# Performance work log

Hardware: AMD Instinct MI355X
Metric: run time of the kernel (lower is better)

## Reference

```python
import jax, jax.numpy as jnp
import numpy as np

NUM_LAYERS = 4
D_MODEL = 128
D_STATE = 16
DELTA_RANK = 8


def setup_inputs() -> dict:
    key = jax.random.key(0)
    ks = jax.random.split(key, 10)
    d, N, dr, L_ = D_MODEL, D_STATE, DELTA_RANK, NUM_LAYERS
    B, R, T = 4, 32, 1024
    x = jax.random.normal(ks[0], (B, R, T), dtype=jnp.float32)

    def w(k, shape, fan_in):
        return jax.random.normal(k, shape, dtype=jnp.float32) / np.sqrt(fan_in).astype(np.float32)

    inp_w = w(ks[1], (d, 1), 1)
    inp_b = jnp.zeros((d,), jnp.float32)
    outp_w = w(ks[2], (1, d), d)
    outp_b = jnp.zeros((1,), jnp.float32)
    ln_g = jnp.ones((L_, d), jnp.float32)
    ln_b = jnp.zeros((L_, d), jnp.float32)
    in_w = w(ks[3], (L_, 2 * d, d), d)
    conv_w = w(ks[4], (L_, d, 3), 3)
    conv_b = jnp.zeros((L_, d), jnp.float32)
    xp_w = w(ks[5], (L_, dr + 2 * N, d), d)
    dp_w = w(ks[6], (L_, d, dr), dr)
    # delta_proj bias = log(dt), dt ~ loguniform(dt_min, dt_max)
    dt = jnp.exp(jax.random.uniform(ks[7], (L_, d), dtype=jnp.float32) * (np.log(0.1) - np.log(0.001)) + np.log(0.001))
    dp_b = jnp.log(dt)
    # A_log = Re(log(-0.5 + i*imag)) = 0.5*log(0.25 + imag^2)
    A_imag = np.arange(1, N + 1, dtype=np.float32) / (1.0 + 2.0 * np.arange(N, dtype=np.float32))
    A_row = 0.5 * np.log(0.25 + A_imag ** 2)
    A_log = jnp.asarray(np.broadcast_to(A_row, (L_, d, N)).copy(), jnp.float32)
    Dp = 0.1 * jnp.ones((L_, d), jnp.float32)
    out_w = w(ks[8], (L_, d, d), d)
    return dict(x=x, inp_w=inp_w, inp_b=inp_b, outp_w=outp_w, outp_b=outp_b,
                ln_g=ln_g, ln_b=ln_b, in_w=in_w, conv_w=conv_w, conv_b=conv_b,
                xp_w=xp_w, dp_w=dp_w, dp_b=dp_b, A_log=A_log, Dp=Dp, out_w=out_w)


def _layernorm(x, g, b):
    mu = jnp.mean(x, -1, keepdims=True)
    v = jnp.var(x, -1, keepdims=True)
    return (x - mu) * jax.lax.rsqrt(v + 1e-5) * g + b


def _selective_scan(u, delta, A_log, Bm, Cm, Dp):
    # u, delta: (Bt, L, d); Bm, Cm: (Bt, L, N); A_log: (d, N); Dp: (d,)
    Bt, L, d = u.shape
    N = A_log.shape[1]
    A = -jnp.exp(A_log)  # (d, N)

    def step(x_prev, inp):
        u_t, dt_t, B_t, C_t = inp  # (Bt,d),(Bt,d),(Bt,N),(Bt,N)
        dA = jnp.exp(dt_t[..., None] * A)                       # (Bt,d,N)
        dBu = dt_t[..., None] * B_t[:, None, :] * u_t[..., None]  # (Bt,d,N)
        x_new = dA * x_prev + dBu
        y_t = jnp.einsum('bdn,bn->bd', x_new, C_t)
        return x_new, y_t

    x0 = jnp.zeros((Bt, d, N), dtype=u.dtype)
    _, ys = jax.lax.scan(step, x0, (u.swapaxes(0, 1), delta.swapaxes(0, 1),
                                    Bm.swapaxes(0, 1), Cm.swapaxes(0, 1)))
    return ys.swapaxes(0, 1) + u * Dp  # (Bt, L, d)


def _block(h, ln_g, ln_b, in_w, conv_w, conv_b, xp_w, dp_w, dp_b, A_log, Dp, out_w):
    Bt, L, d = h.shape
    dr = dp_w.shape[1]
    N = A_log.shape[1]
    z = _layernorm(h, ln_g, ln_b)
    xr = z @ in_w.T                      # (Bt, L, 2d)
    xi, res = jnp.split(xr, 2, axis=-1)
    # depthwise causal conv, kernel=3 (torch pad=2 then crop [:L] == left-pad 2)
    xp = jnp.pad(xi, ((0, 0), (2, 0), (0, 0)))
    xc = (xp[:, 0:L] * conv_w[:, 0] + xp[:, 1:L + 1] * conv_w[:, 1]
          + xp[:, 2:L + 2] * conv_w[:, 2]) + conv_b
    xc = jax.nn.silu(xc)
    dbc = xc @ xp_w.T                    # (Bt, L, dr + 2N)
    dlt, Bm, Cm = jnp.split(dbc, [dr, dr + N], axis=-1)
    delta = jax.nn.softplus(dlt @ dp_w.T + dp_b)  # (Bt, L, d)
    y = _selective_scan(xc, delta, A_log, Bm, Cm, Dp)
    y = y * jax.nn.silu(res)
    return y @ out_w.T


def reference(x, inp_w, inp_b, outp_w, outp_b, ln_g, ln_b, in_w, conv_w, conv_b,
              xp_w, dp_w, dp_b, A_log, Dp, out_w):
    B, R, T = x.shape
    h = x.reshape(B * R, T, 1) @ inp_w.T + inp_b  # (B*R, T, d)
    for i in range(ln_g.shape[0]):
        h = _block(h, ln_g[i], ln_b[i], in_w[i], conv_w[i], conv_b[i], xp_w[i],
                   dp_w[i], dp_b[i], A_log[i], Dp[i], out_w[i]) + h
    out = (h @ outp_w.T + outp_b)[..., 0]  # (B*R, T)
    return out.reshape(B, R, T)
```

## Files before the change

### kernel.cpp

```cpp
#include <hip/hip_runtime.h>
#include <math.h>

#define D 128
#define NSTATE 16
#define DR 8
#define T_SEQ 1024
#define NTOK 131072
#define SEG 16
#define SEGLEN 64
#define ZS 136
#define XRS2 132

typedef __attribute__((ext_vector_type(8))) short bf16x8;
typedef __attribute__((ext_vector_type(4))) float f32x4;

#define LOG2E 1.44269504088896340736f
#define LN2   0.69314718055994530942f

__device__ __forceinline__ float sigmoidf_(float x) {
    return __builtin_amdgcn_rcpf(1.0f + exp2f(-x * LOG2E));
}
__device__ __forceinline__ float softplusf_(float x) {
    float t = LN2 * __builtin_amdgcn_logf(1.0f + exp2f(x * LOG2E));
    return (x > 20.0f) ? x : t;
}
__device__ __forceinline__ short f2bf(float f) {
    union { float f; unsigned u; } v; v.f = f;
    unsigned r = v.u + 0x7FFFu + ((v.u >> 16) & 1u);
    return (short)(r >> 16);
}
__device__ __forceinline__ float bf2f(short s) {
    union { unsigned u; float f; } v; v.u = ((unsigned)(unsigned short)s) << 16;
    return v.f;
}


__global__ void k_prepw(const float* __restrict__ src, short* __restrict__ hi,
                        short* __restrict__ lo, int n) {
    int i = blockIdx.x * 256 + threadIdx.x;
    if (i < n) {
        float f = src[i];
        short hh = f2bf(f);
        hi[i] = hh;
        lo[i] = f2bf(f - bf2f(hh));
    }
}

__global__ void k_prepw_xp(const float* __restrict__ src, short* __restrict__ hi,
                           short* __restrict__ lo) {
    int i = blockIdx.x * 256 + threadIdx.x;
    if (i >= 4 * 48 * 128) return;
    int l = i / (48 * 128);
    int rem = i - l * 48 * 128;
    int j = rem >> 7, k = rem & 127;
    float f = (j < 40) ? src[(l * 40 + j) * 128 + k] : 0.f;
    short hh = f2bf(f);
    hi[i] = hh;
    lo[i] = f2bf(f - bf2f(hh));
}

__global__ void k_a2(const float* __restrict__ A_log, float* __restrict__ A2, int total) {
    int idx = blockIdx.x * blockDim.x + threadIdx.x;
    if (idx < total) A2[idx] = -__expf(A_log[idx]) * LOG2E;
}

__global__ void k_init_h(const float* __restrict__ x, const float* __restrict__ inp_w,
                         const float* __restrict__ inp_b, float* __restrict__ h) {
    int idx = blockIdx.x * blockDim.x + threadIdx.x;
    int tok = idx >> 7;
    int d = idx & 127;
    h[idx] = x[tok] * inp_w[d] + inp_b[d];
}

__global__ __launch_bounds__(256) void k_ln_inproj_conv(
    const float* __restrict__ h, const float* __restrict__ ln_g, const float* __restrict__ ln_b,
    const short* __restrict__ wh, const short* __restrict__ wl,
    const short* __restrict__ xph, const short* __restrict__ xpl,
    const float* __restrict__ conv_w, const float* __restrict__ conv_b,
    float* __restrict__ xc, float* __restrict__ res,
    float* __restrict__ bc, float* __restrict__ dlt)
{
    __shared__ __align__(16) short zsh[48 * ZS];
    __shared__ __align__(16) short zsl[48 * ZS];
    __shared__ __align__(16) float xr[34 * XRS2];
    __shared__ __align__(16) float dbc_l[32][52];
    const int tid = threadIdx.x;
    const int wv = tid >> 6, lane = tid & 63;
    const int tstart = blockIdx.x * 32;
    const int tin = tstart & (T_SEQ - 1);

    for (int r = wv; r < 34; r += 4) {
        int tr = tin + r - 2;
        if (tr < 0) {
            zsh[r * ZS + lane] = 0; zsh[r * ZS + lane + 64] = 0;
            zsl[r * ZS + lane] = 0; zsl[r * ZS + lane + 64] = 0;
            continue;
        }
        size_t row = (size_t)(tstart + r - 2) * D;
        float a = h[row + lane];
        float b = h[row + lane + 64];
        float s = a + b, ss = a * a + b * b;
        #pragma unroll
        for (int m = 1; m < 64; m <<= 1) { s += __shfl_xor(s, m); ss += __shfl_xor(ss, m); }
        float mu = s * (1.0f / 128.0f);
        float var = ss * (1.0f / 128.0f) - mu * mu;
        float rstd = rsqrtf(var + 1e-5f);
        float z0 = (a - mu) * rstd * ln_g[lane]      + ln_b[lane];
        float z1 = (b - mu) * rstd * ln_g[lane + 64] + ln_b[lane + 64];
        short h0 = f2bf(z0), h1 = f2bf(z1);
        zsh[r * ZS + lane]      = h0;
        zsh[r * ZS + lane + 64] = h1;
        zsl[r * ZS + lane]      = f2bf(z0 - bf2f(h0));
        zsl[r * ZS + lane + 64] = f2bf(z1 - bf2f(h1));
    }
    for (int i = tid; i < 14 * 128; i += 256) {
        int r = 34 + (i >> 7), c = i & 127;
        zsh[r * ZS + c] = 0;
        zsl[r * ZS + c] = 0;
    }

    const int colb = wv * 64 + (lane & 15);
    const int kb = (lane >> 4) * 8;
    bf16x8 bw[4][4];
    #pragma unroll
    for (int ct = 0; ct < 4; ++ct)
        #pragma unroll
        for (int kf = 0; kf < 4; ++kf)
            bw[ct][kf] = *(const bf16x8*)&wh[(colb + ct * 16) * 128 + kf * 32 + kb];
    __syncthreads();

    f32x4 acc[3][4];
    #pragma unroll
    for (int b = 0; b < 3; ++b)
        #pragma unroll
        for (int ct = 0; ct < 4; ++ct)
            acc[b][ct] = (f32x4){0.f, 0.f, 0.f, 0.f};

    #pragma unroll
    for (int b = 0; b < 3; ++b) {
        bf16x8 ah[4], al[4];
        const int rbase = (b * 16 + (lane & 15)) * ZS + kb;
        #pragma unroll
        for (int kf = 0; kf < 4; ++kf) {
            ah[kf] = *(const bf16x8*)&zsh[rbase + kf * 32];
            al[kf] = *(const bf16x8*)&zsl[rbase + kf * 32];
        }
        #pragma unroll
        for (int ct = 0; ct < 4; ++ct)
            #pragma unroll
            for (int kf = 0; kf < 4; ++kf) {
                acc[b][ct] = __builtin_amdgcn_mfma_f32_16x16x32_bf16(ah[kf], bw[ct][kf], acc[b][ct], 0, 0, 0);
                acc[b][ct] = __builtin_amdgcn_mfma_f32_16x16x32_bf16(al[kf], bw[ct][kf], acc[b][ct], 0, 0, 0);
            }
    }
    #pragma unroll
    for (int ct = 0; ct < 4; ++ct)
        #pragma unroll
        for (int kf = 0; kf < 4; ++kf)
            bw[ct][kf] = *(const bf16x8*)&wl[(colb + ct * 16) * 128 + kf * 32 + kb];
    #pragma unroll
    for (int b = 0; b < 3; ++b) {
        bf16x8 ah[4];
        const int rbase = (b * 16 + (lane & 15)) * ZS + kb;
        #pragma unroll
        for (int kf = 0; kf < 4; ++kf)
            ah[kf] = *(const bf16x8*)&zsh[rbase + kf * 32];
        #pragma unroll
        for (int ct = 0; ct < 4; ++ct)
            #pragma unroll
            for (int kf = 0; kf < 4; ++kf)
                acc[b][ct] = __builtin_amdgcn_mfma_f32_16x16x32_bf16(ah[kf], bw[ct][kf], acc[b][ct], 0, 0, 0);
    }

    if (wv < 2) {
        #pragma unroll
        for (int b = 0; b < 3; ++b)
            #pragma unroll
            for (int ct = 0; ct < 4; ++ct) {
                const int col = wv * 64 + ct * 16 + (lane & 15);
                #pragma unroll
                for (int i = 0; i < 4; ++i) {
                    int row = b * 16 + ((lane >> 4) << 2) + i;
                    if (row < 34) xr[row * XRS2 + col] = acc[b][ct][i];
                }
            }
    }
    __syncthreads();

    {
        int ch = tid & 127, s0 = (tid >> 7) * 16;
        float c0 = conv_w[ch * 3 + 0], c1 = conv_w[ch * 3 + 1], c2 = conv_w[ch * 3 + 2];
        float cb = conv_b[ch];
        float v0 = xr[(s0 + 0) * XRS2 + ch], v1 = xr[(s0 + 1) * XRS2 + ch];
        #pragma unroll
        for (int s = 0; s < 16; ++s) {
            float v2 = xr[(s0 + s + 2) * XRS2 + ch];
            float v = v0 * c0 + v1 * c1 + v2 * c2 + cb;
            v = v * sigmoidf_(v);
            xc[(size_t)(tstart + s0 + s) * D + ch] = v;
            short hh = f2bf(v);
            zsh[(s0 + s) * ZS + ch] = hh;
            zsl[(s0 + s) * ZS + ch] = f2bf(v - bf2f(hh));
            v0 = v1; v1 = v2;
        }
    }
    __syncthreads();

    if (wv >= 2) {
        #pragma unroll
        for (int b = 0; b < 3; ++b)
            #pragma unroll
            for (int ct = 0; ct < 4; ++ct) {
                const int col = (wv - 2) * 64 + ct * 16 + (lane & 15);
                #pragma unroll
                for (int i = 0; i < 4; ++i) {
                    int row = b * 16 + ((lane >> 4) << 2) + i;
                    if (row >= 2 && row < 34) xr[row * XRS2 + col] = acc[b][ct][i];
                }
            }
    }
    for (int tile = wv; tile < 6; tile += 4) {
        const int b = tile & 1, ct = tile >> 1;
        const int jcol = ct * 16 + (lane & 15);
        const int rbase = (b * 16 + (lane & 15)) * ZS + kb;
        bf16x8 ah[4], al[4], bh[4];
        #pragma unroll
        for (int kf = 0; kf < 4; ++kf) {
            ah[kf] = *(const bf16x8*)&zsh[rbase + kf * 32];
            al[kf] = *(const bf16x8*)&zsl[rbase + kf * 32];
            bh[kf] = *(const bf16x8*)&xph[jcol * 128 + kf * 32 + kb];
        }
        f32x4 a2 = (f32x4){0.f, 0.f, 0.f, 0.f};
        #pragma unroll
        for (int kf = 0; kf < 4; ++kf) {
            a2 = __builtin_amdgcn_mfma_f32_16x16x32_bf16(ah[kf], bh[kf], a2, 0, 0, 0);
            a2 = __builtin_amdgcn_mfma_f32_16x16x32_bf16(al[kf], bh[kf], a2, 0, 0, 0);
        }
        #pragma unroll
        for (int kf = 0; kf < 4; ++kf) {
            bh[kf] = *(const bf16x8*)&xpl[jcol * 128 + kf * 32 + kb];
            a2 = __builtin_amdgcn_mfma_f32_16x16x32_bf16(ah[kf], bh[kf], a2, 0, 0, 0);
        }
        #pragma unroll
        for (int i = 0; i < 4; ++i) {
            int t = b * 16 + ((lane >> 4) << 2) + i;
            dbc_l[t][jcol] = a2[i];
        }
    }
    __syncthreads();

    for (int fi = tid; fi < 1024; fi += 256) {
        int r = fi >> 5, c4 = fi & 31;
        *(float4*)&res[(size_t)(tstart + r) * D + c4 * 4] =
            *(const float4*)&xr[(r + 2) * XRS2 + c4 * 4];
    }
    {
        int t = tid >> 3, q = tid & 7;
        *(float4*)&bc[(size_t)(tstart + t) * 32 + q * 4] = *(const float4*)&dbc_l[t][8 + q * 4];
    }
    if (tid < 64) {
        int t = tid >> 1, j4 = tid & 1;
        *(float4*)&dlt[(size_t)(tstart + t) * 8 + j4 * 4] = *(const float4*)&dbc_l[t][j4 * 4];
    }
}

__global__ __launch_bounds__(256) void k_scan1(
    const float* __restrict__ xc, const float* __restrict__ bc,
    const float* __restrict__ dlt,
    const float* __restrict__ dp_w, const float* __restrict__ dp_b,
    const float* __restrict__ A2,
    float* __restrict__ Sbuf, float* __restrict__ Fbuf)
{
    const int tid = threadIdx.x;
    const int d = tid & 127;
    const int segid = blockIdx.x * 2 + (tid >> 7);
    const size_t segbase = (size_t)segid * SEGLEN;

    float dpw[DR];
    #pragma unroll
    for (int r = 0; r < DR; ++r) dpw[r] = dp_w[d * DR + r];
    const float dpb = dp_b[d];
    float A2r[NSTATE];
    #pragma unroll
    for (int n = 0; n < NSTATE; ++n) A2r[n] = A2[d * NSTATE + n];
    float xs[NSTATE];
    #pragma unroll
    for (int n = 0; n < NSTATE; ++n) xs[n] = 0.f;
    float S = 0.f;

    float4 dl0 = *(const float4*)&dlt[segbase * 8];
    float4 dl1 = *(const float4*)&dlt[segbase * 8 + 4];
    float4 B0 = *(const float4*)&bc[segbase * 32 + 0];
    float4 B1 = *(const float4*)&bc[segbase * 32 + 4];
    float4 B2 = *(const float4*)&bc[segbase * 32 + 8];
    float4 B3 = *(const float4*)&bc[segbase * 32 + 12];
    float uv = xc[segbase * D + d];

    for (int tl = 0; tl < SEGLEN; ++tl) {
        float4 cd0 = dl0, cd1 = dl1, cB0 = B0, cB1 = B1, cB2 = B2, cB3 = B3;
        float cu = uv;
        if (tl + 1 < SEGLEN) {
            const size_t nt = segbase + tl + 1;
            dl0 = *(const float4*)&dlt[nt * 8];
            dl1 = *(const float4*)&dlt[nt * 8 + 4];
            B0 = *(const float4*)&bc[nt * 32 + 0];
            B1 = *(const float4*)&bc[nt * 32 + 4];
            B2 = *(const float4*)&bc[nt * 32 + 8];
            B3 = *(const float4*)&bc[nt * 32 + 12];
            uv = xc[nt * D + d];
        }
        float v = dpb;
        v = fmaf(cd0.x, dpw[0], v); v = fmaf(cd0.y, dpw[1], v);
        v = fmaf(cd0.z, dpw[2], v); v = fmaf(cd0.w, dpw[3], v);
        v = fmaf(cd1.x, dpw[4], v); v = fmaf(cd1.y, dpw[5], v);
        v = fmaf(cd1.z, dpw[6], v); v = fmaf(cd1.w, dpw[7], v);
        float dt = softplusf_(v);
        float duv = dt * cu;
        S += dt;
        xs[0]  = fmaf(exp2f(dt * A2r[0]),  xs[0],  duv * cB0.x);
        xs[1]  = fmaf(exp2f(dt * A2r[1]),  xs[1],  duv * cB0.y);
        xs[2]  = fmaf(exp2f(dt * A2r[2]),  xs[2],  duv * cB0.z);
        xs[3]  = fmaf(exp2f(dt * A2r[3]),  xs[3],  duv * cB0.w);
        xs[4]  = fmaf(exp2f(dt * A2r[4]),  xs[4],  duv * cB1.x);
        xs[5]  = fmaf(exp2f(dt * A2r[5]),  xs[5],  duv * cB1.y);
        xs[6]  = fmaf(exp2f(dt * A2r[6]),  xs[6],  duv * cB1.z);
        xs[7]  = fmaf(exp2f(dt * A2r[7]),  xs[7],  duv * cB1.w);
        xs[8]  = fmaf(exp2f(dt * A2r[8]),  xs[8],  duv * cB2.x);
        xs[9]  = fmaf(exp2f(dt * A2r[9]),  xs[9],  duv * cB2.y);
        xs[10] = fmaf(exp2f(dt * A2r[10]), xs[10], duv * cB2.z);
        xs[11] = fmaf(exp2f(dt * A2r[11]), xs[11], duv * cB2.w);
        xs[12] = fmaf(exp2f(dt * A2r[12]), xs[12], duv * cB3.x);
        xs[13] = fmaf(exp2f(dt * A2r[13]), xs[13], duv * cB3.y);
        xs[14] = fmaf(exp2f(dt * A2r[14]), xs[14], duv * cB3.z);
        xs[15] = fmaf(exp2f(dt * A2r[15]), xs[15], duv * cB3.w);
    }
    const size_t o = ((size_t)segid * D + d) * NSTATE;
    #pragma unroll
    for (int nq = 0; nq < 4; ++nq)
        *(float4*)&Fbuf[o + nq * 4] =
            make_float4(xs[nq*4], xs[nq*4+1], xs[nq*4+2], xs[nq*4+3]);
    Sbuf[(size_t)segid * D + d] = S;
}

__global__ __launch_bounds__(256) void k_scan2(
    const float* __restrict__ xc, const float* __restrict__ bc,
    const float* __restrict__ dlt,
    const float* __restrict__ dp_w, const float* __restrict__ dp_b,
    const float* __restrict__ A2, const float* __restrict__ Dp,
    const float* __restrict__ Sbuf, const float* __restrict__ Fbuf,
    float* __restrict__ resy)
{
    const int tid = threadIdx.x;
    const int d = tid & 127;
    const int segid = blockIdx.x * 2 + (tid >> 7);
    const int seg = segid & (SEG - 1);
    const int seg0 = segid - seg;
    const size_t segbase = (size_t)segid * SEGLEN;

    float dpw[DR];
    #pragma unroll
    for (int r = 0; r < DR; ++r) dpw[r] = dp_w[d * DR + r];
    const float dpb = dp_b[d];
    float A2r[NSTATE];
    #pragma unroll
    for (int n = 0; n < NSTATE; ++n) A2r[n] = A2[d * NSTATE + n];
    const float Dpd = Dp[d];

    float xs[NSTATE];
    #pragma unroll
    for (int n = 0; n < NSTATE; ++n) xs[n] = 0.f;
    for (int s = 0; s < seg; ++s) {
        const int sid = seg0 + s;
        const float Sv = Sbuf[(size_t)sid * D + d];
        const size_t idx = ((size_t)sid * D + d) * NSTATE;
        #pragma unroll
        for (int n = 0; n < NSTATE; ++n) {
            float F = Fbuf[idx + n];
            xs[n] = fmaf(exp2f(A2r[n] * Sv), xs[n], F);
        }
    }

    float4 dl0 = *(const float4*)&dlt[segbase * 8];
    float4 dl1 = *(const float4*)&dlt[segbase * 8 + 4];
    float4 B0 = *(const float4*)&bc[segbase * 32 + 0];
    float4 B1 = *(const float4*)&bc[segbase * 32 + 4];
    float4 B2 = *(const float4*)&bc[segbase * 32 + 8];
    float4 B3 = *(const float4*)&bc[segbase * 32 + 12];
    float4 C0 = *(const float4*)&bc[segbase * 32 + 16];
    float4 C1 = *(const float4*)&bc[segbase * 32 + 20];
    float4 C2 = *(const float4*)&bc[segbase * 32 + 24];
    float4 C3 = *(const float4*)&bc[segbase * 32 + 28];
    float uv = xc[segbase * D + d];
    float rg = resy[segbase * D + d];

    for (int tl = 0; tl < SEGLEN; ++tl) {
        float4 cd0 = dl0, cd1 = dl1;
        float4 cB0 = B0, cB1 = B1, cB2 = B2, cB3 = B3;
        float4 cC0 = C0, cC1 = C1, cC2 = C2, cC3 = C3;
        float cu = uv, cg = rg;
        if (tl + 1 < SEGLEN) {
            const size_t nt = segbase + tl + 1;
            dl0 = *(const float4*)&dlt[nt * 8];
            dl1 = *(const float4*)&dlt[nt * 8 + 4];
            B0 = *(const float4*)&bc[nt * 32 + 0];
            B1 = *(const float4*)&bc[nt * 32 + 4];
            B2 = *(const float4*)&bc[nt * 32 + 8];
            B3 = *(const float4*)&bc[nt * 32 + 12];
            C0 = *(const float4*)&bc[nt * 32 + 16];
            C1 = *(const float4*)&bc[nt * 32 + 20];
            C2 = *(const float4*)&bc[nt * 32 + 24];
            C3 = *(const float4*)&bc[nt * 32 + 28];
            uv = xc[nt * D + d];
            rg = resy[nt * D + d];
        }
        float v = dpb;
        v = fmaf(cd0.x, dpw[0], v); v = fmaf(cd0.y, dpw[1], v);
        v = fmaf(cd0.z, dpw[2], v); v = fmaf(cd0.w, dpw[3], v);
        v = fmaf(cd1.x, dpw[4], v); v = fmaf(cd1.y, dpw[5], v);
        v = fmaf(cd1.z, dpw[6], v); v = fmaf(cd1.w, dpw[7], v);
        float dt = softplusf_(v);
        float duv = dt * cu;
        xs[0]  = fmaf(exp2f(dt * A2r[0]),  xs[0],  duv * cB0.x);
        xs[1]  = fmaf(exp2f(dt * A2r[1]),  xs[1],  duv * cB0.y);
        xs[2]  = fmaf(exp2f(dt * A2r[2]),  xs[2],  duv * cB0.z);
        xs[3]  = fmaf(exp2f(dt * A2r[3]),  xs[3],  duv * cB0.w);
        xs[4]  = fmaf(exp2f(dt * A2r[4]),  xs[4],  duv * cB1.x);
        xs[5]  = fmaf(exp2f(dt * A2r[5]),  xs[5],  duv * cB1.y);
        xs[6]  = fmaf(exp2f(dt * A2r[6]),  xs[6],  duv * cB1.z);
        xs[7]  = fmaf(exp2f(dt * A2r[7]),  xs[7],  duv * cB1.w);
        xs[8]  = fmaf(exp2f(dt * A2r[8]),  xs[8],  duv * cB2.x);
        xs[9]  = fmaf(exp2f(dt * A2r[9]),  xs[9],  duv * cB2.y);
        xs[10] = fmaf(exp2f(dt * A2r[10]), xs[10], duv * cB2.z);
        xs[11] = fmaf(exp2f(dt * A2r[11]), xs[11], duv * cB2.w);
        xs[12] = fmaf(exp2f(dt * A2r[12]), xs[12], duv * cB3.x);
        xs[13] = fmaf(exp2f(dt * A2r[13]), xs[13], duv * cB3.y);
        xs[14] = fmaf(exp2f(dt * A2r[14]), xs[14], duv * cB3.z);
        xs[15] = fmaf(exp2f(dt * A2r[15]), xs[15], duv * cB3.w);
        float y = xs[0] * cC0.x;
        y = fmaf(xs[1],  cC0.y, y);
        y = fmaf(xs[2],  cC0.z, y);
        y = fmaf(xs[3],  cC0.w, y);
        y = fmaf(xs[4],  cC1.x, y);
        y = fmaf(xs[5],  cC1.y, y);
        y = fmaf(xs[6],  cC1.z, y);
        y = fmaf(xs[7],  cC1.w, y);
        y = fmaf(xs[8],  cC2.x, y);
        y = fmaf(xs[9],  cC2.y, y);
        y = fmaf(xs[10], cC2.z, y);
        y = fmaf(xs[11], cC2.w, y);
        y = fmaf(xs[12], cC3.x, y);
        y = fmaf(xs[13], cC3.y, y);
        y = fmaf(xs[14], cC3.z, y);
        y = fmaf(xs[15], cC3.w, y);
        y = fmaf(cu, Dpd, y);
        resy[(segbase + tl) * D + d] = y * (cg * sigmoidf_(cg));
    }
}

__global__ __launch_bounds__(256) void k_outproj(
    const float* __restrict__ y, const short* __restrict__ wh, const short* __restrict__ wl,
    float* __restrict__ h)
{
    __shared__ __align__(16) short ysh[32 * ZS];
    __shared__ __align__(16) short ysl[32 * ZS];
    const int tid = threadIdx.x;
    const int wv = tid >> 6, lane = tid & 63;
    const size_t tb = (size_t)blockIdx.x * 32;

    #pragma unroll
    for (int i = 0; i < 4; ++i) {
        int idx = tid + i * 256;
        int row = idx >> 5, c4 = idx & 31;
        float4 v = *(const float4*)&y[(tb + row) * D + c4 * 4];
        short h0 = f2bf(v.x), h1 = f2bf(v.y), h2 = f2bf(v.z), h3 = f2bf(v.w);
        *(short4*)&ysh[row * ZS + c4 * 4] = make_short4(h0, h1, h2, h3);
        *(short4*)&ysl[row * ZS + c4 * 4] = make_short4(
            f2bf(v.x - bf2f(h0)), f2bf(v.y - bf2f(h1)),
            f2bf(v.z - bf2f(h2)), f2bf(v.w - bf2f(h3)));
    }

    const int colb = wv * 32 + (lane & 15);
    const int kb = (lane >> 4) * 8;
    bf16x8 bw[2][4];
    #pragma unroll
    for (int ct = 0; ct < 2; ++ct)
        #pragma unroll
        for (int kf = 0; kf < 4; ++kf)
            bw[ct][kf] = *(const bf16x8*)&wh[(colb + ct * 16) * 128 + kf * 32 + kb];
    __syncthreads();

    f32x4 acc[2][2];
    #pragma unroll
    for (int b = 0; b < 2; ++b)
        #pragma unroll
        for (int ct = 0; ct < 2; ++ct)
            acc[b][ct] = (f32x4){0.f, 0.f, 0.f, 0.f};

    #pragma unroll
    for (int b = 0; b < 2; ++b) {
        bf16x8 ah[4], al[4];
        const int rbase = (b * 16 + (lane & 15)) * ZS + kb;
        #pragma unroll
        for (int kf = 0; kf < 4; ++kf) {
            ah[kf] = *(const bf16x8*)&ysh[rbase + kf * 32];
            al[kf] = *(const bf16x8*)&ysl[rbase + kf * 32];
        }
        #pragma unroll
        for (int ct = 0; ct < 2; ++ct)
            #pragma unroll
            for (int kf = 0; kf < 4; ++kf) {
                acc[b][ct] = __builtin_amdgcn_mfma_f32_16x16x32_bf16(ah[kf], bw[ct][kf], acc[b][ct], 0, 0, 0);
                acc[b][ct] = __builtin_amdgcn_mfma_f32_16x16x32_bf16(al[kf], bw[ct][kf], acc[b][ct], 0, 0, 0);
            }
    }
    #pragma unroll
    for (int ct = 0; ct < 2; ++ct)
        #pragma unroll
        for (int kf = 0; kf < 4; ++kf)
            bw[ct][kf] = *(const bf16x8*)&wl[(colb + ct * 16) * 128 + kf * 32 + kb];
    #pragma unroll
    for (int b = 0; b < 2; ++b) {
        bf16x8 ah[4];
        const int rbase = (b * 16 + (lane & 15)) * ZS + kb;
        #pragma unroll
        for (int kf = 0; kf < 4; ++kf)
            ah[kf] = *(const bf16x8*)&ysh[rbase + kf * 32];
        #pragma unroll
        for (int ct = 0; ct < 2; ++ct)
            #pragma unroll
            for (int kf = 0; kf < 4; ++kf)
                acc[b][ct] = __builtin_amdgcn_mfma_f32_16x16x32_bf16(ah[kf], bw[ct][kf], acc[b][ct], 0, 0, 0);
    }

    #pragma unroll
    for (int b = 0; b < 2; ++b)
        #pragma unroll
        for (int ct = 0; ct < 2; ++ct) {
            const int col = wv * 32 + ct * 16 + (lane & 15);
            #pragma unroll
            for (int i = 0; i < 4; ++i) {
                int row = b * 16 + ((lane >> 4) << 2) + i;
                size_t o = (tb + row) * D + col;
                h[o] += acc[b][ct][i];
            }
        }
}

__global__ __launch_bounds__(256) void k_final(
    const float* __restrict__ h, const float* __restrict__ outp_w,
    const float* __restrict__ outp_b, float* __restrict__ out)
{
    const int tid = threadIdx.x;
    const int lane = tid & 63;
    const size_t tok = (size_t)blockIdx.x * 4 + (tid >> 6);
    float a = h[tok * D + lane] * outp_w[lane] + h[tok * D + lane + 64] * outp_w[lane + 64];
    #pragma unroll
    for (int m = 1; m < 64; m <<= 1) a += __shfl_xor(a, m);
    if (lane == 0) out[tok] = a + outp_b[0];
}

extern "C" void kernel_launch(void* const* d_in, const int* in_sizes, int n_in,
                              void* d_out, int out_size, void* d_ws, size_t ws_size,
                              hipStream_t stream)
{
    const float* x      = (const float*)d_in[0];
    const float* inp_w  = (const float*)d_in[1];
    const float* inp_b  = (const float*)d_in[2];
    const float* outp_w = (const float*)d_in[3];
    const float* outp_b = (const float*)d_in[4];
    const float* ln_g   = (const float*)d_in[5];
    const float* ln_b   = (const float*)d_in[6];
    const float* in_w   = (const float*)d_in[7];
    const float* conv_w = (const float*)d_in[8];
    const float* conv_b = (const float*)d_in[9];
    const float* xp_w   = (const float*)d_in[10];
    const float* dp_w   = (const float*)d_in[11];
    const float* dp_b   = (const float*)d_in[12];
    const float* A_log  = (const float*)d_in[13];
    const float* Dp     = (const float*)d_in[14];
    const float* out_w  = (const float*)d_in[15];

    float* ws = (float*)d_ws;
    size_t off = 0;
    float* h      = ws + off; off += (size_t)NTOK * D;
    float* xc     = ws + off; off += (size_t)NTOK * D;
    float* resy   = ws + off; off += (size_t)NTOK * D;
    float* bc     = ws + off; off += (size_t)NTOK * 32;
    float* dlt    = ws + off; off += (size_t)NTOK * 8;
    float* Fbuf   = ws + off; off += 128 * SEG * 2048;
    float* Sbuf   = ws + off; off += 128 * SEG * 128;
    short* in_wBh = (short*)(ws + off); off += 4 * 256 * 128 / 2;
    short* in_wBl = (short*)(ws + off); off += 4 * 256 * 128 / 2;
    short* out_wBh= (short*)(ws + off); off += 4 * 128 * 128 / 2;
    short* out_wBl= (short*)(ws + off); off += 4 * 128 * 128 / 2;
    short* xp_wBh = (short*)(ws + off); off += 4 * 48 * 128 / 2;
    short* xp_wBl = (short*)(ws + off); off += 4 * 48 * 128 / 2;
    float* A2     = ws + off; off += 4 * 128 * 16;
    if (ws_size < off * sizeof(float)) return;

    k_prepw<<<(4 * 256 * 128 + 255) / 256, 256, 0, stream>>>(in_w, in_wBh, in_wBl, 4 * 256 * 128);
    k_prepw<<<(4 * 128 * 128 + 255) / 256, 256, 0, stream>>>(out_w, out_wBh, out_wBl, 4 * 128 * 128);
    k_prepw_xp<<<(4 * 48 * 128 + 255) / 256, 256, 0, stream>>>(xp_w, xp_wBh, xp_wBl);
    k_a2<<<(4 * 128 * 16 + 255) / 256, 256, 0, stream>>>(A_log, A2, 4 * 128 * 16);
    k_init_h<<<NTOK * D / 256, 256, 0, stream>>>(x, inp_w, inp_b, h);

    for (int l = 0; l < 4; ++l) {
        k_ln_inproj_conv<<<NTOK / 32, 256, 0, stream>>>(
            h, ln_g + l * 128, ln_b + l * 128,
            in_wBh + l * 256 * 128, in_wBl + l * 256 * 128,
            xp_wBh + l * 48 * 128, xp_wBl + l * 48 * 128,
            conv_w + l * 128 * 3, conv_b + l * 128, xc, resy, bc, dlt);
        k_scan1<<<1024, 256, 0, stream>>>(xc, bc, dlt, dp_w + l * 128 * 8, dp_b + l * 128,
                                          A2 + l * 128 * 16, Sbuf, Fbuf);
        k_scan2<<<1024, 256, 0, stream>>>(xc, bc, dlt, dp_w + l * 128 * 8, dp_b + l * 128,
                                          A2 + l * 128 * 16, Dp + l * 128, Sbuf, Fbuf, resy);
        k_outproj<<<NTOK / 32, 256, 0, stream>>>(resy, out_wBh + l * 128 * 128,
                                                 out_wBl + l * 128 * 128, h);
    }
    k_final<<<NTOK / 4, 256, 0, stream>>>(h, outp_w, outp_b, (float*)d_out);
}
```

Baseline: 1.584 ms.

## Split scan state dimension across thread pairs to double scan parallelism

Both scan kernels now assign each (segment, channel) to two threads, each owning half of the 16 SSM states, with a shuffle-xor reducing the output dot product. The grid doubles to 2048 blocks of one segment each. This halves per-thread serial work and register pressure to improve latency hiding and occupancy. The cost is softplus and delta-projection work done twice per channel, more duplicated dlt/xc loads, and an extra shuffle per step.

```diff
diff --git a/kernel.cpp b/kernel.cpp
--- a/kernel.cpp
+++ b/kernel.cpp
@@ -272,41 +272,38 @@
     float* __restrict__ Sbuf, float* __restrict__ Fbuf)
 {
     const int tid = threadIdx.x;
-    const int d = tid & 127;
-    const int segid = blockIdx.x * 2 + (tid >> 7);
+    const int d = tid >> 1;
+    const int nh = tid & 1;
+    const int segid = blockIdx.x;
     const size_t segbase = (size_t)segid * SEGLEN;
 
     float dpw[DR];
     #pragma unroll
     for (int r = 0; r < DR; ++r) dpw[r] = dp_w[d * DR + r];
     const float dpb = dp_b[d];
-    float A2r[NSTATE];
-    #pragma unroll
-    for (int n = 0; n < NSTATE; ++n) A2r[n] = A2[d * NSTATE + n];
-    float xs[NSTATE];
-    #pragma unroll
-    for (int n = 0; n < NSTATE; ++n) xs[n] = 0.f;
+    float A2r[8];
+    #pragma unroll
+    for (int n = 0; n < 8; ++n) A2r[n] = A2[d * NSTATE + nh * 8 + n];
+    float xs[8];
+    #pragma unroll
+    for (int n = 0; n < 8; ++n) xs[n] = 0.f;
     float S = 0.f;
 
     float4 dl0 = *(const float4*)&dlt[segbase * 8];
     float4 dl1 = *(const float4*)&dlt[segbase * 8 + 4];
-    float4 B0 = *(const float4*)&bc[segbase * 32 + 0];
-    float4 B1 = *(const float4*)&bc[segbase * 32 + 4];
-    float4 B2 = *(const float4*)&bc[segbase * 32 + 8];
-    float4 B3 = *(const float4*)&bc[segbase * 32 + 12];
+    float4 B0 = *(const float4*)&bc[segbase * 32 + nh * 8 + 0];
+    float4 B1 = *(const float4*)&bc[segbase * 32 + nh * 8 + 4];
     float uv = xc[segbase * D + d];
 
     for (int tl = 0; tl < SEGLEN; ++tl) {
-        float4 cd0 = dl0, cd1 = dl1, cB0 = B0, cB1 = B1, cB2 = B2, cB3 = B3;
+        float4 cd0 = dl0, cd1 = dl1, cB0 = B0, cB1 = B1;
         float cu = uv;
         if (tl + 1 < SEGLEN) {
             const size_t nt = segbase + tl + 1;
             dl0 = *(const float4*)&dlt[nt * 8];
             dl1 = *(const float4*)&dlt[nt * 8 + 4];
-            B0 = *(const float4*)&bc[nt * 32 + 0];
-            B1 = *(const float4*)&bc[nt * 32 + 4];
-            B2 = *(const float4*)&bc[nt * 32 + 8];
-            B3 = *(const float4*)&bc[nt * 32 + 12];
+            B0 = *(const float4*)&bc[nt * 32 + nh * 8 + 0];
+            B1 = *(const float4*)&bc[nt * 32 + nh * 8 + 4];
             uv = xc[nt * D + d];
         }
         float v = dpb;
@@ -317,29 +314,19 @@
         float dt = softplusf_(v);
         float duv = dt * cu;
         S += dt;
-        xs[0]  = fmaf(exp2f(dt * A2r[0]),  xs[0],  duv * cB0.x);
-        xs[1]  = fmaf(exp2f(dt * A2r[1]),  xs[1],  duv * cB0.y);
-        xs[2]  = fmaf(exp2f(dt * A2r[2]),  xs[2],  duv * cB0.z);
-        xs[3]  = fmaf(exp2f(dt * A2r[3]),  xs[3],  duv * cB0.w);
-        xs[4]  = fmaf(exp2f(dt * A2r[4]),  xs[4],  duv * cB1.x);
-        xs[5]  = fmaf(exp2f(dt * A2r[5]),  xs[5],  duv * cB1.y);
-        xs[6]  = fmaf(exp2f(dt * A2r[6]),  xs[6],  duv * cB1.z);
-        xs[7]  = fmaf(exp2f(dt * A2r[7]),  xs[7],  duv * cB1.w);
-        xs[8]  = fmaf(exp2f(dt * A2r[8]),  xs[8],  duv * cB2.x);
-        xs[9]  = fmaf(exp2f(dt * A2r[9]),  xs[9],  duv * cB2.y);
-        xs[10] = fmaf(exp2f(dt * A2r[10]), xs[10], duv * cB2.z);
-        xs[11] = fmaf(exp2f(dt * A2r[11]), xs[11], duv * cB2.w);
-        xs[12] = fmaf(exp2f(dt * A2r[12]), xs[12], duv * cB3.x);
-        xs[13] = fmaf(exp2f(dt * A2r[13]), xs[13], duv * cB3.y);
-        xs[14] = fmaf(exp2f(dt * A2r[14]), xs[14], duv * cB3.z);
-        xs[15] = fmaf(exp2f(dt * A2r[15]), xs[15], duv * cB3.w);
-    }
-    const size_t o = ((size_t)segid * D + d) * NSTATE;
-    #pragma unroll
-    for (int nq = 0; nq < 4; ++nq)
-        *(float4*)&Fbuf[o + nq * 4] =
-            make_float4(xs[nq*4], xs[nq*4+1], xs[nq*4+2], xs[nq*4+3]);
-    Sbuf[(size_t)segid * D + d] = S;
+        xs[0] = fmaf(exp2f(dt * A2r[0]), xs[0], duv * cB0.x);
+        xs[1] = fmaf(exp2f(dt * A2r[1]), xs[1], duv * cB0.y);
+        xs[2] = fmaf(exp2f(dt * A2r[2]), xs[2], duv * cB0.z);
+        xs[3] = fmaf(exp2f(dt * A2r[3]), xs[3], duv * cB0.w);
+        xs[4] = fmaf(exp2f(dt * A2r[4]), xs[4], duv * cB1.x);
+        xs[5] = fmaf(exp2f(dt * A2r[5]), xs[5], duv * cB1.y);
+        xs[6] = fmaf(exp2f(dt * A2r[6]), xs[6], duv * cB1.z);
+        xs[7] = fmaf(exp2f(dt * A2r[7]), xs[7], duv * cB1.w);
+    }
+    const size_t o = ((size_t)segid * D + d) * NSTATE + nh * 8;
+    *(float4*)&Fbuf[o + 0] = make_float4(xs[0], xs[1], xs[2], xs[3]);
+    *(float4*)&Fbuf[o + 4] = make_float4(xs[4], xs[5], xs[6], xs[7]);
+    if (nh == 0) Sbuf[(size_t)segid * D + d] = S;
 }
 
 __global__ __launch_bounds__(256) void k_scan2(
@@ -351,8 +338,9 @@
     float* __restrict__ resy)
 {
     const int tid = threadIdx.x;
-    const int d = tid & 127;
-    const int segid = blockIdx.x * 2 + (tid >> 7);
+    const int d = tid >> 1;
+    const int nh = tid & 1;
+    const int segid = blockIdx.x;
     const int seg = segid & (SEG - 1);
     const int seg0 = segid - seg;
     const size_t segbase = (size_t)segid * SEGLEN;
@@ -361,55 +349,51 @@
     #pragma unroll
     for (int r = 0; r < DR; ++r) dpw[r] = dp_w[d * DR + r];
     const float dpb = dp_b[d];
-    float A2r[NSTATE];
-    #pragma unroll
-    for (int n = 0; n < NSTATE; ++n) A2r[n] = A2[d * NSTATE + n];
+    float A2r[8];
+    #pragma unroll
+    for (int n = 0; n < 8; ++n) A2r[n] = A2[d * NSTATE + nh * 8 + n];
     const float Dpd = Dp[d];
 
-    float xs[NSTATE];
-    #pragma unroll
-    for (int n = 0; n < NSTATE; ++n) xs[n] = 0.f;
+    float xs[8];
+    #pragma unroll
+    for (int n = 0; n < 8; ++n) xs[n] = 0.f;
     for (int s = 0; s < seg; ++s) {
         const int sid = seg0 + s;
         const float Sv = Sbuf[(size_t)sid * D + d];
-        const size_t idx = ((size_t)sid * D + d) * NSTATE;
-        #pragma unroll
-        for (int n = 0; n < NSTATE; ++n) {
-            float F = Fbuf[idx + n];
-            xs[n] = fmaf(exp2f(A2r[n] * Sv), xs[n], F);
-        }
+        const size_t idx = ((size_t)sid * D + d) * NSTATE + nh * 8;
+        float4 F0 = *(const float4*)&Fbuf[idx + 0];
+        float4 F1 = *(const float4*)&Fbuf[idx + 4];
+        xs[0] = fmaf(exp2f(A2r[0] * Sv), xs[0], F0.x);
+        xs[1] = fmaf(exp2f(A2r[1] * Sv), xs[1], F0.y);
+        xs[2] = fmaf(exp2f(A2r[2] * Sv), xs[2], F0.z);
+        xs[3] = fmaf(exp2f(A2r[3] * Sv), xs[3], F0.w);
+        xs[4] = fmaf(exp2f(A2r[4] * Sv), xs[4], F1.x);
+        xs[5] = fmaf(exp2f(A2r[5] * Sv), xs[5], F1.y);
+        xs[6] = fmaf(exp2f(A2r[6] * Sv), xs[6], F1.z);
+        xs[7] = fmaf(exp2f(A2r[7] * Sv), xs[7], F1.w);
     }
 
     float4 dl0 = *(const float4*)&dlt[segbase * 8];
     float4 dl1 = *(const float4*)&dlt[segbase * 8 + 4];
-    float4 B0 = *(const float4*)&bc[segbase * 32 + 0];
-    float4 B1 = *(const float4*)&bc[segbase * 32 + 4];
-    float4 B2 = *(const float4*)&bc[segbase * 32 + 8];
-    float4 B3 = *(const float4*)&bc[segbase * 32 + 12];
-    float4 C0 = *(const float4*)&bc[segbase * 32 + 16];
-    float4 C1 = *(const float4*)&bc[segbase * 32 + 20];
-    float4 C2 = *(const float4*)&bc[segbase * 32 + 24];
-    float4 C3 = *(const float4*)&bc[segbase * 32 + 28];
+    float4 B0 = *(const float4*)&bc[segbase * 32 + nh * 8 + 0];
+    float4 B1 = *(const float4*)&bc[segbase * 32 + nh * 8 + 4];
+    float4 C0 = *(const float4*)&bc[segbase * 32 + 16 + nh * 8 + 0];
+    float4 C1 = *(const float4*)&bc[segbase * 32 + 16 + nh * 8 + 4];
     float uv = xc[segbase * D + d];
     float rg = resy[segbase * D + d];
 
     for (int tl = 0; tl < SEGLEN; ++tl) {
         float4 cd0 = dl0, cd1 = dl1;
-        float4 cB0 = B0, cB1 = B1, cB2 = B2, cB3 = B3;
-        float4 cC0 = C0, cC1 = C1, cC2 = C2, cC3 = C3;
+        float4 cB0 = B0, cB1 = B1, cC0 = C0, cC1 = C1;
         float cu = uv, cg = rg;
         if (tl + 1 < SEGLEN) {
             const size_t nt = segbase + tl + 1;
             dl0 = *(const float4*)&dlt[nt * 8];
             dl1 = *(const float4*)&dlt[nt * 8 + 4];
-            B0 = *(const float4*)&bc[nt * 32 + 0];
-            B1 = *(const float4*)&bc[nt * 32 + 4];
-            B2 = *(const float4*)&bc[nt * 32 + 8];
-            B3 = *(const float4*)&bc[nt * 32 + 12];
-            C0 = *(const float4*)&bc[nt * 32 + 16];
-            C1 = *(const float4*)&bc[nt * 32 + 20];
-            C2 = *(const float4*)&bc[nt * 32 + 24];
-            C3 = *(const float4*)&bc[nt * 32 + 28];
+            B0 = *(const float4*)&bc[nt * 32 + nh * 8 + 0];
+            B1 = *(const float4*)&bc[nt * 32 + nh * 8 + 4];
+            C0 = *(const float4*)&bc[nt * 32 + 16 + nh * 8 + 0];
+            C1 = *(const float4*)&bc[nt * 32 + 16 + nh * 8 + 4];
             uv = xc[nt * D + d];
             rg = resy[nt * D + d];
         }
@@ -420,40 +404,27 @@
         v = fmaf(cd1.z, dpw[6], v); v = fmaf(cd1.w, dpw[7], v);
         float dt = softplusf_(v);
         float duv = dt * cu;
-        xs[0]  = fmaf(exp2f(dt * A2r[0]),  xs[0],  duv * cB0.x);
-        xs[1]  = fmaf(exp2f(dt * A2r[1]),  xs[1],  duv * cB0.y);
-        xs[2]  = fmaf(exp2f(dt * A2r[2]),  xs[2],  duv * cB0.z);
-        xs[3]  = fmaf(exp2f(dt * A2r[3]),  xs[3],  duv * cB0.w);
-        xs[4]  = fmaf(exp2f(dt * A2r[4]),  xs[4],  duv * cB1.x);
-        xs[5]  = fmaf(exp2f(dt * A2r[5]),  xs[5],  duv * cB1.y);
-        xs[6]  = fmaf(exp2f(dt * A2r[6]),  xs[6],  duv * cB1.z);
-        xs[7]  = fmaf(exp2f(dt * A2r[7]),  xs[7],  duv * cB1.w);
-        xs[8]  = fmaf(exp2f(dt * A2r[8]),  xs[8],  duv * cB2.x);
-        xs[9]  = fmaf(exp2f(dt * A2r[9]),  xs[9],  duv * cB2.y);
-        xs[10] = fmaf(exp2f(dt * A2r[10]), xs[10], duv * cB2.z);
-        xs[11] = fmaf(exp2f(dt * A2r[11]), xs[11], duv * cB2.w);
-        xs[12] = fmaf(exp2f(dt * A2r[12]), xs[12], duv * cB3.x);
-        xs[13] = fmaf(exp2f(dt * A2r[13]), xs[13], duv * cB3.y);
-        xs[14] = fmaf(exp2f(dt * A2r[14]), xs[14], duv * cB3.z);
-        xs[15] = fmaf(exp2f(dt * A2r[15]), xs[15], duv * cB3.w);
+        xs[0] = fmaf(exp2f(dt * A2r[0]), xs[0], duv * cB0.x);
+        xs[1] = fmaf(exp2f(dt * A2r[1]), xs[1], duv * cB0.y);
+        xs[2] = fmaf(exp2f(dt * A2r[2]), xs[2], duv * cB0.z);
+        xs[3] = fmaf(exp2f(dt * A2r[3]), xs[3], duv * cB0.w);
+        xs[4] = fmaf(exp2f(dt * A2r[4]), xs[4], duv * cB1.x);
+        xs[5] = fmaf(exp2f(dt * A2r[5]), xs[5], duv * cB1.y);
+        xs[6] = fmaf(exp2f(dt * A2r[6]), xs[6], duv * cB1.z);
+        xs[7] = fmaf(exp2f(dt * A2r[7]), xs[7], duv * cB1.w);
         float y = xs[0] * cC0.x;
-        y = fmaf(xs[1],  cC0.y, y);
-        y = fmaf(xs[2],  cC0.z, y);
-        y = fmaf(xs[3],  cC0.w, y);
-        y = fmaf(xs[4],  cC1.x, y);
-        y = fmaf(xs[5],  cC1.y, y);
-        y = fmaf(xs[6],  cC1.z, y);
-        y = fmaf(xs[7],  cC1.w, y);
-        y = fmaf(xs[8],  cC2.x, y);
-        y = fmaf(xs[9],  cC2.y, y);
-        y = fmaf(xs[10], cC2.z, y);
-        y = fmaf(xs[11], cC2.w, y);
-        y = fmaf(xs[12], cC3.x, y);
-        y = fmaf(xs[13], cC3.y, y);
-        y = fmaf(xs[14], cC3.z, y);
-        y = fmaf(xs[15], cC3.w, y);
-        y = fmaf(cu, Dpd, y);
-        resy[(segbase + tl) * D + d] = y * (cg * sigmoidf_(cg));
+        y = fmaf(xs[1], cC0.y, y);
+        y = fmaf(xs[2], cC0.z, y);
+        y = fmaf(xs[3], cC0.w, y);
+        y = fmaf(xs[4], cC1.x, y);
+        y = fmaf(xs[5], cC1.y, y);
+        y = fmaf(xs[6], cC1.z, y);
+        y = fmaf(xs[7], cC1.w, y);
+        y += __shfl_xor(y, 1);
+        if (nh == 0) {
+            y = fmaf(cu, Dpd, y);
+            resy[(segbase + tl) * D + d] = y * (cg * sigmoidf_(cg));
+        }
     }
 }
 
@@ -610,9 +581,9 @@
             in_wBh + l * 256 * 128, in_wBl + l * 256 * 128,
             xp_wBh + l * 48 * 128, xp_wBl + l * 48 * 128,
             conv_w + l * 128 * 3, conv_b + l * 128, xc, resy, bc, dlt);
-        k_scan1<<<1024, 256, 0, stream>>>(xc, bc, dlt, dp_w + l * 128 * 8, dp_b + l * 128,
+        k_scan1<<<2048, 256, 0, stream>>>(xc, bc, dlt, dp_w + l * 128 * 8, dp_b + l * 128,
                                           A2 + l * 128 * 16, Sbuf, Fbuf);
-        k_scan2<<<1024, 256, 0, stream>>>(xc, bc, dlt, dp_w + l * 128 * 8, dp_b + l * 128,
+        k_scan2<<<2048, 256, 0, stream>>>(xc, bc, dlt, dp_w + l * 128 * 8, dp_b + l * 128,
                                           A2 + l * 128 * 16, Dp + l * 128, Sbuf, Fbuf, resy);
         k_outproj<<<NTOK / 32, 256, 0, stream>>>(resy, out_wBh + l * 128 * 128,
                                                  out_wBl + l * 128 * 128, h);
```

Result: no change. 1.565 ms (-1.2%).
